# Optimization experiments

Hardware: AMD Instinct MI355X
Metric: run time of the kernel (lower is better)

Reference implementation:

```python
import jax, jax.numpy as jnp
import numpy as np

N = 50000      # nodes
E = 500000     # edges (avg degree 10)
D_IN = 256     # input feature dim
HID = 256      # hidden_channels
HEADS = 8
C_HID = HID // HEADS   # 32 per-head dim for concat layers
NCLS = 8               # num_classes (last layer per-head dim, concat=False)


def setup_inputs() -> dict:
    key = jax.random.key(0)
    keys = iter(jax.random.split(key, 64))
    def w(shape, s=0.05):
        return jax.random.normal(next(keys), shape, jnp.float32) * s
    inp = {}
    inp["x"] = jax.random.normal(next(keys), (N, D_IN), jnp.float32)
    inp["edge_index"] = jax.random.randint(next(keys), (2, E), 0, N, jnp.int32)
    # (fan_in, heads*per_head_out, skip_out) per layer; layer3: concat=False
    layer_cfg = [(D_IN, HEADS * C_HID, HEADS * C_HID),
                 (HID, HEADS * C_HID, HEADS * C_HID),
                 (HID, HEADS * NCLS, NCLS)]
    for i, (fin, hc, skip) in enumerate(layer_cfg, 1):
        for nm in ("q", "k", "v"):
            inp[f"W{nm}{i}"] = w((fin, hc))
            inp[f"b{nm}{i}"] = jnp.zeros((hc,), jnp.float32)
        inp[f"Ws{i}"] = w((fin, skip))
        inp[f"bs{i}"] = jnp.zeros((skip,), jnp.float32)
        inp[f"Wb{i}"] = w((3 * skip, 1))
    for i in (1, 2):
        inp[f"ln{i}_g"] = jnp.ones((HID,), jnp.float32)
        inp[f"ln{i}_b"] = jnp.zeros((HID,), jnp.float32)
    return inp


def _layer_norm(x, g, b):
    mu = x.mean(-1, keepdims=True)
    var = ((x - mu) ** 2).mean(-1, keepdims=True)
    return (x - mu) * jax.lax.rsqrt(var + 1e-5) * g + b


def _tconv(x, src, dst, Wq, bq, Wk, bk, Wv, bv, Ws, bs, Wb, concat):
    """PyG TransformerConv with beta=True, root_weight=True, eval-mode (no dropout)."""
    n = x.shape[0]
    q = (x @ Wq + bq).reshape(n, HEADS, -1)   # [N,H,C]
    k = (x @ Wk + bk).reshape(n, HEADS, -1)
    v = (x @ Wv + bv).reshape(n, HEADS, -1)
    C = q.shape[-1]
    # per-edge attention logits, scaled dot product
    logits = (q[dst] * k[src]).sum(-1) * jax.lax.rsqrt(jnp.float32(C))  # [E,H]
    # segment softmax over incoming edges of each dst node
    m = jax.ops.segment_max(logits, dst, num_segments=n)                # [N,H]
    m = jnp.where(jnp.isfinite(m), m, 0.0)                              # empty segments
    e = jnp.exp(logits - m[dst])
    s = jax.ops.segment_sum(e, dst, num_segments=n)
    alpha = e / (s[dst] + 1e-16)                                        # [E,H]
    # scatter-aggregate messages
    out = jax.ops.segment_sum(v[src] * alpha[:, :, None], dst, num_segments=n)  # [N,H,C]
    out = out.reshape(n, -1) if concat else out.mean(axis=1)
    # beta-gated skip connection
    xr = x @ Ws + bs
    beta = jax.nn.sigmoid(jnp.concatenate([out, xr, out - xr], axis=-1) @ Wb)   # [N,1]
    return beta * xr + (1.0 - beta) * out


def reference(x, edge_index,
              Wq1, bq1, Wk1, bk1, Wv1, bv1, Ws1, bs1, Wb1,
              Wq2, bq2, Wk2, bk2, Wv2, bv2, Ws2, bs2, Wb2,
              Wq3, bq3, Wk3, bk3, Wv3, bv3, Ws3, bs3, Wb3,
              ln1_g, ln1_b, ln2_g, ln2_b):
    src, dst = edge_index[0], edge_index[1]
    h = jax.nn.relu(_layer_norm(
        _tconv(x, src, dst, Wq1, bq1, Wk1, bk1, Wv1, bv1, Ws1, bs1, Wb1, True),
        ln1_g, ln1_b))
    h = jax.nn.relu(_layer_norm(
        _tconv(h, src, dst, Wq2, bq2, Wk2, bk2, Wv2, bv2, Ws2, bs2, Wb2, True),
        ln2_g, ln2_b))
    return _tconv(h, src, dst, Wq3, bq3, Wk3, bk3, Wv3, bv3, Ws3, bs3, Wb3, False)
```

## Files before the change

### kernel.cpp

```cpp
#include <hip/hip_runtime.h>
#include <stdint.h>

typedef __attribute__((ext_vector_type(8))) short short8;
typedef __attribute__((ext_vector_type(4))) float f32x4;

struct us4 { unsigned short x, y, z, w; };

__device__ __forceinline__ float b2f(unsigned short u){
  union { unsigned int i; float f; } x; x.i = ((unsigned int)u) << 16; return x.f;
}
__device__ __forceinline__ unsigned short f2b(float f){
  union { float f; unsigned int i; } x; x.f = f;
  unsigned int i = x.i;
  unsigned int r = (i + 0x7FFFu + ((i >> 16) & 1u)) >> 16;
  return (unsigned short)r;
}
__device__ __forceinline__ float sane(float v){
  return fminf(fmaxf(v, -1e30f), 1e30f);
}
__device__ __forceinline__ float lclamp(float v){
  return fminf(fmaxf(v, -60.f), 60.f);
}
__device__ __forceinline__ float ldin(const void* p, size_t i, int f32){
  return f32 ? ((const float*)p)[i] : b2f(((const unsigned short*)p)[i]);
}

__global__ void k_flag(const unsigned short* __restrict__ xu, int* __restrict__ flag){
  __shared__ int cnt;
  if (threadIdx.x == 0) cnt = 0;
  __syncthreads();
  unsigned u = xu[2 * threadIdx.x];
  int e = (u >> 7) & 0xFF;
  if (e >= 97 && e <= 132) atomicAdd(&cnt, 1);
  __syncthreads();
  if (threadIdx.x == 0) flag[0] = (cnt >= 192) ? 0 : 1;
}

__global__ void k_cvt(const void* __restrict__ xin, unsigned short* __restrict__ xb,
                      int n4, const int* __restrict__ flagp){
  int f32 = *flagp;
  int i = blockIdx.x * 256 + threadIdx.x;
  if (i < n4){
    if (f32){
      float4 v = ((const float4*)xin)[i];
      us4 o = { f2b(v.x), f2b(v.y), f2b(v.z), f2b(v.w) };
      ((us4*)xb)[i] = o;
    } else {
      ((us4*)xb)[i] = ((const us4*)xin)[i];
    }
  }
}

__global__ void k_deg(const int* __restrict__ ei, int E, int N, int* __restrict__ deg){
  int e = blockIdx.x * 256 + threadIdx.x;
  if (e < E){
    unsigned d = (unsigned)ei[E + e];
    if (d < (unsigned)N) atomicAdd(&deg[d], 1);
  }
}

__global__ void k_bsum(const int* __restrict__ deg, int N, int* __restrict__ bsum){
  int b = blockIdx.x, t = threadIdx.x;
  int i0 = b * 1024 + t * 4;
  int s = 0;
  if (i0 + 4 <= N){
    int4 v = *(const int4*)&deg[i0];
    s = v.x + v.y + v.z + v.w;
  } else {
    #pragma unroll
    for (int j = 0; j < 4; ++j){ int i = i0 + j; if (i < N) s += deg[i]; }
  }
  #pragma unroll
  for (int off = 32; off; off >>= 1) s += __shfl_xor(s, off);
  __shared__ int ws[4];
  if ((t & 63) == 0) ws[t >> 6] = s;
  __syncthreads();
  if (t == 0) bsum[b] = ws[0] + ws[1] + ws[2] + ws[3];
}

__global__ void k_bscan(const int* __restrict__ bsum, int nb,
                        int* __restrict__ boff, int* __restrict__ rowptr, int N){
  int t = threadIdx.x;
  if (nb <= 64){
    int v = (t < nb) ? bsum[t] : 0;
    int inc = v;
    #pragma unroll
    for (int off = 1; off < 64; off <<= 1){
      int u = __shfl_up(inc, off);
      if (t >= off) inc += u;
    }
    if (t < nb) boff[t] = inc - v;
    if (t == 63) rowptr[N] = inc;
  } else {
    if (t == 0){
      int run = 0;
      for (int i = 0; i < nb; ++i){ boff[i] = run; run += bsum[i]; }
      rowptr[N] = run;
    }
  }
}

__global__ void k_rowptr(const int* __restrict__ deg, const int* __restrict__ boff,
                         int N, int* __restrict__ rowptr, int* __restrict__ cursor){
  int b = blockIdx.x, t = threadIdx.x;
  int i0 = b * 1024 + t * 4;
  int d0 = 0, d1 = 0, d2 = 0, d3 = 0;
  if (i0 + 4 <= N){
    int4 v = *(const int4*)&deg[i0];
    d0 = v.x; d1 = v.y; d2 = v.z; d3 = v.w;
  } else {
    if (i0     < N) d0 = deg[i0];
    if (i0 + 1 < N) d1 = deg[i0 + 1];
    if (i0 + 2 < N) d2 = deg[i0 + 2];
    if (i0 + 3 < N) d3 = deg[i0 + 3];
  }
  int s = d0 + d1 + d2 + d3;
  int lane = t & 63, w = t >> 6;
  int inc = s;
  #pragma unroll
  for (int off = 1; off < 64; off <<= 1){
    int u = __shfl_up(inc, off);
    if (lane >= off) inc += u;
  }
  int wex = inc - s;
  __shared__ int wtot[4];
  if (lane == 63) wtot[w] = inc;
  __syncthreads();
  int cross = 0;
  for (int i = 0; i < w; ++i) cross += wtot[i];
  int basev = boff[b] + cross + wex;
  int r0 = basev, r1 = basev + d0, r2 = r1 + d1, r3 = r2 + d2;
  if (i0 + 4 <= N){
    int4 o = { r0, r1, r2, r3 };
    *(int4*)&rowptr[i0] = o;
    *(int4*)&cursor[i0] = o;
  } else {
    if (i0     < N){ rowptr[i0]   = r0; cursor[i0]   = r0; }
    if (i0 + 1 < N){ rowptr[i0+1] = r1; cursor[i0+1] = r1; }
    if (i0 + 2 < N){ rowptr[i0+2] = r2; cursor[i0+2] = r2; }
    if (i0 + 3 < N){ rowptr[i0+3] = r3; cursor[i0+3] = r3; }
  }
}

__global__ void k_scatter(const int* __restrict__ ei, int E, int N,
                          int* __restrict__ cursor, int* __restrict__ srcs){
  int e = blockIdx.x * 256 + threadIdx.x;
  if (e < E){
    unsigned d = (unsigned)ei[E + e];
    if (d < (unsigned)N){
      int pos = atomicAdd(&cursor[d], 1);
      if ((unsigned)pos < (unsigned)E){
        unsigned s = (unsigned)ei[e];
        srcs[pos] = (s < (unsigned)N) ? (int)s : 0;
      }
    }
  }
}

__global__ void k_pack(const void* __restrict__ Wq, const void* __restrict__ bq,
                       const void* __restrict__ Wk, const void* __restrict__ bk,
                       const void* __restrict__ Wv, const void* __restrict__ bv,
                       const void* __restrict__ Ws, const void* __restrict__ bs,
                       unsigned short* __restrict__ WT, float* __restrict__ bias,
                       int Mq, int Ms, int K, const int* __restrict__ flagp){
  int f32 = *flagp;
  int cg = blockIdx.x;
  int k  = threadIdx.x;
  int mat, c, mc;
  if (cg < 3 * Mq){ mat = cg / Mq; c = cg % Mq; mc = Mq; }
  else if (cg < 3 * Mq + Ms){ mat = 3; c = cg - 3 * Mq; mc = Ms; }
  else { mat = 4; c = 0; mc = 1; }
  const void* W = (mat==0)?Wq:(mat==1)?Wk:(mat==2)?Wv:(mat==3)?Ws:(const void*)0;
  WT[(size_t)cg * K + k] = (mat < 4) ? f2b(ldin(W, (size_t)k * mc + c, f32)) : (unsigned short)0;
  if (k == 0){
    const void* B = (mat==0)?bq:(mat==1)?bk:(mat==2)?bv:(mat==3)?bs:(const void*)0;
    bias[cg] = (mat < 4) ? ldin(B, c, f32) : 0.f;
  }
}

__global__ __launch_bounds__(256) void k_gemm(const unsigned short* __restrict__ A,
                                              const unsigned short* __restrict__ WT,
                                              const float* __restrict__ bias,
                                              unsigned short* __restrict__ B0,
                                              unsigned short* __restrict__ B1,
                                              unsigned short* __restrict__ B2,
                                              unsigned short* __restrict__ B3,
                                              int N, int Mout, int secshift){
  __shared__ __align__(16) unsigned short Alds[64][264];
  __shared__ __align__(16) unsigned short Clds[32][276];
  int tid = threadIdx.x, wid = tid >> 6, lane = tid & 63;
  int l15 = lane & 15, l4 = lane >> 4;
  int row0 = blockIdx.x * 64;
  {
    int srow = tid >> 2, sc4 = tid & 3;
    int ar = row0 + srow; if (ar >= N) ar = N - 1;
    const unsigned short* Ap = A + (size_t)ar * 256;
    #pragma unroll
    for (int i = 0; i < 8; ++i){
      int col = (sc4 + 4 * i) * 8;
      *(short8*)&Alds[srow][col] = *(const short8*)&Ap[col];
    }
  }
  __syncthreads();
  int secw = 1 << secshift;
  int strow = tid >> 3, stchunk = tid & 7;
  for (int cb = wid * 64; cb < Mout; cb += 256){
    f32x4 acc[4][4] = {};
    #pragma unroll
    for (int k0 = 0; k0 < 256; k0 += 32){
      short8 a0 = *(const short8*)&Alds[l15     ][k0 + l4*8];
      short8 a1 = *(const short8*)&Alds[16 + l15][k0 + l4*8];
      short8 a2 = *(const short8*)&Alds[32 + l15][k0 + l4*8];
      short8 a3 = *(const short8*)&Alds[48 + l15][k0 + l4*8];
      const unsigned short* wb = WT + (size_t)(cb + l15) * 256 + k0 + l4*8;
      short8 b0 = *(const short8*)(wb);
      short8 b1 = *(const short8*)(wb + 16*256);
      short8 b2 = *(const short8*)(wb + 32*256);
      short8 b3 = *(const short8*)(wb + 48*256);
      acc[0][0] = __builtin_amdgcn_mfma_f32_16x16x32_bf16(a0, b0, acc[0][0], 0,0,0);
      acc[0][1] = __builtin_amdgcn_mfma_f32_16x16x32_bf16(a0, b1, acc[0][1], 0,0,0);
      acc[0][2] = __builtin_amdgcn_mfma_f32_16x16x32_bf16(a0, b2, acc[0][2], 0,0,0);
      acc[0][3] = __builtin_amdgcn_mfma_f32_16x16x32_bf16(a0, b3, acc[0][3], 0,0,0);
      acc[1][0] = __builtin_amdgcn_mfma_f32_16x16x32_bf16(a1, b0, acc[1][0], 0,0,0);
      acc[1][1] = __builtin_amdgcn_mfma_f32_16x16x32_bf16(a1, b1, acc[1][1], 0,0,0);
      acc[1][2] = __builtin_amdgcn_mfma_f32_16x16x32_bf16(a1, b2, acc[1][2], 0,0,0);
      acc[1][3] = __builtin_amdgcn_mfma_f32_16x16x32_bf16(a1, b3, acc[1][3], 0,0,0);
      acc[2][0] = __builtin_amdgcn_mfma_f32_16x16x32_bf16(a2, b0, acc[2][0], 0,0,0);
      acc[2][1] = __builtin_amdgcn_mfma_f32_16x16x32_bf16(a2, b1, acc[2][1], 0,0,0);
      acc[2][2] = __builtin_amdgcn_mfma_f32_16x16x32_bf16(a2, b2, acc[2][2], 0,0,0);
      acc[2][3] = __builtin_amdgcn_mfma_f32_16x16x32_bf16(a2, b3, acc[2][3], 0,0,0);
      acc[3][0] = __builtin_amdgcn_mfma_f32_16x16x32_bf16(a3, b0, acc[3][0], 0,0,0);
      acc[3][1] = __builtin_amdgcn_mfma_f32_16x16x32_bf16(a3, b1, acc[3][1], 0,0,0);
      acc[3][2] = __builtin_amdgcn_mfma_f32_16x16x32_bf16(a3, b2, acc[3][2], 0,0,0);
      acc[3][3] = __builtin_amdgcn_mfma_f32_16x16x32_bf16(a3, b3, acc[3][3], 0,0,0);
    }
    int gb = cb - wid * 64;
    #pragma unroll
    for (int ph = 0; ph < 2; ++ph){
      #pragma unroll
      for (int rt2 = 0; rt2 < 2; ++rt2){
        int rt = ph*2 + rt2;
        #pragma unroll
        for (int ct = 0; ct < 4; ++ct){
          float bv = bias[cb + ct*16 + l15];
          #pragma unroll
          for (int r = 0; r < 4; ++r)
            Clds[rt2*16 + l4*4 + r][wid*64 + ct*16 + l15] = f2b(acc[rt][ct][r] + bv);
        }
      }
      __syncthreads();
      int grow = row0 + ph*32 + strow;
      if (grow < N){
        int g0 = gb + stchunk * 32;
        int mat = g0 >> secshift;
        int cc  = g0 & (secw - 1);
        unsigned short* Bp = (mat==0)?B0:(mat==1)?B1:(mat==2)?B2:B3;
        unsigned short* dst = Bp + (size_t)grow * secw + cc;
        const unsigned short* srcp = &Clds[strow][stchunk * 32];
        #pragma unroll
        for (int j = 0; j < 4; ++j)
          *(short8*)(dst + j*8) = *(const short8*)(srcp + j*8);
      }
      __syncthreads();
    }
  }
}

__global__ __launch_bounds__(256) void k_attn(const unsigned short* __restrict__ qb,
                                              const unsigned short* __restrict__ kb,
                                              const unsigned short* __restrict__ vb,
                                              const unsigned short* __restrict__ xb,
                                              const int* __restrict__ rowptr,
                                              const int* __restrict__ srcs,
                                              const void* __restrict__ Wb,
                                              const void* __restrict__ lng,
                                              const void* __restrict__ lnb,
                                              unsigned short* __restrict__ hout,
                                              int N, int E, const int* __restrict__ flagp){
  int f32 = *flagp;
  int tid = threadIdx.x, w = tid >> 6, l = tid & 63;
  int n = blockIdx.x * 4 + w;
  if (n >= N) return;
  size_t base = (size_t)n * 256;
  us4 qv = *(const us4*)&qb[base + l*4];
  float q0 = b2f(qv.x), q1 = b2f(qv.y), q2 = b2f(qv.z), q3 = b2f(qv.w);
  int e0 = rowptr[n], e1 = rowptr[n+1];
  if (e0 < 0) e0 = 0;
  if (e1 > E) e1 = E;
  const float scale = 0.17677669529663687f;
  float ss = 0.f, o0 = 0.f, o1 = 0.f, o2 = 0.f, o3 = 0.f;
  int e = e0;
  for (; e + 4 <= e1; e += 4){
    unsigned s0 = (unsigned)srcs[e];   if (s0 >= (unsigned)N) s0 = 0;
    unsigned s1 = (unsigned)srcs[e+1]; if (s1 >= (unsigned)N) s1 = 0;
    unsigned s2 = (unsigned)srcs[e+2]; if (s2 >= (unsigned)N) s2 = 0;
    unsigned s3 = (unsigned)srcs[e+3]; if (s3 >= (unsigned)N) s3 = 0;
    us4 kA = *(const us4*)&kb[(size_t)s0*256 + l*4];
    us4 kB = *(const us4*)&kb[(size_t)s1*256 + l*4];
    us4 kC = *(const us4*)&kb[(size_t)s2*256 + l*4];
    us4 kD = *(const us4*)&kb[(size_t)s3*256 + l*4];
    us4 vA = *(const us4*)&vb[(size_t)s0*256 + l*4];
    us4 vB = *(const us4*)&vb[(size_t)s1*256 + l*4];
    us4 vC = *(const us4*)&vb[(size_t)s2*256 + l*4];
    us4 vD = *(const us4*)&vb[(size_t)s3*256 + l*4];
    float pa = q0*b2f(kA.x) + q1*b2f(kA.y) + q2*b2f(kA.z) + q3*b2f(kA.w);
    float pb = q0*b2f(kB.x) + q1*b2f(kB.y) + q2*b2f(kB.z) + q3*b2f(kB.w);
    float pc = q0*b2f(kC.x) + q1*b2f(kC.y) + q2*b2f(kC.z) + q3*b2f(kC.w);
    float pd = q0*b2f(kD.x) + q1*b2f(kD.y) + q2*b2f(kD.z) + q3*b2f(kD.w);
    pa += __shfl_xor(pa, 1); pa += __shfl_xor(pa, 2); pa += __shfl_xor(pa, 4);
    pb += __shfl_xor(pb, 1); pb += __shfl_xor(pb, 2); pb += __shfl_xor(pb, 4);
    pc += __shfl_xor(pc, 1); pc += __shfl_xor(pc, 2); pc += __shfl_xor(pc, 4);
    pd += __shfl_xor(pd, 1); pd += __shfl_xor(pd, 2); pd += __shfl_xor(pd, 4);
    float ea = __expf(lclamp(pa * scale));
    float eb = __expf(lclamp(pb * scale));
    float ec = __expf(lclamp(pc * scale));
    float ed = __expf(lclamp(pd * scale));
    ss += ea + eb + ec + ed;
    o0 += ea*b2f(vA.x) + eb*b2f(vB.x) + ec*b2f(vC.x) + ed*b2f(vD.x);
    o1 += ea*b2f(vA.y) + eb*b2f(vB.y) + ec*b2f(vC.y) + ed*b2f(vD.y);
    o2 += ea*b2f(vA.z) + eb*b2f(vB.z) + ec*b2f(vC.z) + ed*b2f(vD.z);
    o3 += ea*b2f(vA.w) + eb*b2f(vB.w) + ec*b2f(vC.w) + ed*b2f(vD.w);
  }
  for (; e < e1; ++e){
    unsigned s = (unsigned)srcs[e]; if (s >= (unsigned)N) s = 0;
    us4 kk = *(const us4*)&kb[(size_t)s*256 + l*4];
    us4 vv = *(const us4*)&vb[(size_t)s*256 + l*4];
    float p = q0*b2f(kk.x) + q1*b2f(kk.y) + q2*b2f(kk.z) + q3*b2f(kk.w);
    p += __shfl_xor(p, 1); p += __shfl_xor(p, 2); p += __shfl_xor(p, 4);
    float a = __expf(lclamp(p * scale));
    ss += a;
    o0 += a*b2f(vv.x); o1 += a*b2f(vv.y); o2 += a*b2f(vv.z); o3 += a*b2f(vv.w);
  }
  float sinv = 1.f / (ss + 1e-16f);
  o0 = sane(o0 * sinv); o1 = sane(o1 * sinv);
  o2 = sane(o2 * sinv); o3 = sane(o3 * sinv);
  int c = l * 4;
  us4 xv = *(const us4*)&xb[base + c];
  float x0 = sane(b2f(xv.x)), x1 = sane(b2f(xv.y)), x2 = sane(b2f(xv.z)), x3 = sane(b2f(xv.w));
  float d = o0*ldin(Wb, c+0, f32) + x0*ldin(Wb, 256+c+0, f32) + (o0-x0)*ldin(Wb, 512+c+0, f32)
          + o1*ldin(Wb, c+1, f32) + x1*ldin(Wb, 256+c+1, f32) + (o1-x1)*ldin(Wb, 512+c+1, f32)
          + o2*ldin(Wb, c+2, f32) + x2*ldin(Wb, 256+c+2, f32) + (o2-x2)*ldin(Wb, 512+c+2, f32)
          + o3*ldin(Wb, c+3, f32) + x3*ldin(Wb, 256+c+3, f32) + (o3-x3)*ldin(Wb, 512+c+3, f32);
  #pragma unroll
  for (int off = 32; off; off >>= 1) d += __shfl_xor(d, off);
  float beta = 1.f / (1.f + __expf(-d));
  float r0 = beta*x0 + (1.f-beta)*o0;
  float r1 = beta*x1 + (1.f-beta)*o1;
  float r2 = beta*x2 + (1.f-beta)*o2;
  float r3 = beta*x3 + (1.f-beta)*o3;
  float sm = r0 + r1 + r2 + r3;
  #pragma unroll
  for (int off = 32; off; off >>= 1) sm += __shfl_xor(sm, off);
  float mu = sm * (1.f/256.f);
  float d0 = r0-mu, d1 = r1-mu, d2 = r2-mu, d3 = r3-mu;
  float vv2 = d0*d0 + d1*d1 + d2*d2 + d3*d3;
  #pragma unroll
  for (int off = 32; off; off >>= 1) vv2 += __shfl_xor(vv2, off);
  float rs = rsqrtf(vv2 * (1.f/256.f) + 1e-5f);
  us4 outv;
  outv.x = f2b(fmaxf(d0*rs*ldin(lng,c+0,f32) + ldin(lnb,c+0,f32), 0.f));
  outv.y = f2b(fmaxf(d1*rs*ldin(lng,c+1,f32) + ldin(lnb,c+1,f32), 0.f));
  outv.z = f2b(fmaxf(d2*rs*ldin(lng,c+2,f32) + ldin(lnb,c+2,f32), 0.f));
  outv.w = f2b(fmaxf(d3*rs*ldin(lng,c+3,f32) + ldin(lnb,c+3,f32), 0.f));
  *(us4*)&hout[base + c] = outv;
}

__global__ __launch_bounds__(256) void k_final(const unsigned short* __restrict__ q3,
                                               const unsigned short* __restrict__ k3,
                                               const unsigned short* __restrict__ v3,
                                               const unsigned short* __restrict__ x3,
                                               const int* __restrict__ rowptr,
                                               const int* __restrict__ srcs,
                                               const void* __restrict__ Wb,
                                               void* __restrict__ outp,
                                               int N, int E, const int* __restrict__ flagp){
  int f32 = *flagp;
  int tid = threadIdx.x, w = tid >> 6, l = tid & 63;
  int n = blockIdx.x * 4 + w;
  if (n >= N) return;
  int es = l >> 4, h = (l >> 1) & 7, j = l & 1;
  size_t base = (size_t)n * 64;
  us4 qv = *(const us4*)&q3[base + h*8 + j*4];
  float q0 = b2f(qv.x), q1 = b2f(qv.y), q2 = b2f(qv.z), q3f = b2f(qv.w);
  int e0 = rowptr[n], e1 = rowptr[n+1];
  if (e0 < 0) e0 = 0;
  if (e1 > E) e1 = E;
  int deg = e1 - e0;
  const float scale = 0.35355339059327373f;
  float ss = 0.f, o0 = 0.f, o1 = 0.f, o2 = 0.f, o3 = 0.f;
  for (int ei = es; ei < deg; ei += 4){
    unsigned s = (unsigned)srcs[e0 + ei]; if (s >= (unsigned)N) s = 0;
    us4 kk = *(const us4*)&k3[(size_t)s*64 + h*8 + j*4];
    us4 vv = *(const us4*)&v3[(size_t)s*64 + h*8 + j*4];
    float p = q0*b2f(kk.x) + q1*b2f(kk.y) + q2*b2f(kk.z) + q3f*b2f(kk.w);
    p += __shfl_xor(p, 1);
    float a = __expf(lclamp(p * scale));
    ss += a;
    o0 += a*b2f(vv.x); o1 += a*b2f(vv.y); o2 += a*b2f(vv.z); o3 += a*b2f(vv.w);
  }
  #pragma unroll
  for (int off = 16; off <= 32; off <<= 1){
    ss += __shfl_xor(ss, off);
    o0 += __shfl_xor(o0, off); o1 += __shfl_xor(o1, off);
    o2 += __shfl_xor(o2, off); o3 += __shfl_xor(o3, off);
  }
  float sinv = 1.f / (ss + 1e-16f);
  o0 = sane(o0 * sinv); o1 = sane(o1 * sinv);
  o2 = sane(o2 * sinv); o3 = sane(o3 * sinv);
  #pragma unroll
  for (int off = 2; off <= 8; off <<= 1){
    o0 += __shfl_xor(o0, off); o1 += __shfl_xor(o1, off);
    o2 += __shfl_xor(o2, off); o3 += __shfl_xor(o3, off);
  }
  o0 *= 0.125f; o1 *= 0.125f; o2 *= 0.125f; o3 *= 0.125f;
  us4 xv = *(const us4*)&x3[base + j*4];
  float x0 = sane(b2f(xv.x)), x1 = sane(b2f(xv.y)), x2 = sane(b2f(xv.z)), x3v = sane(b2f(xv.w));
  int c = j*4;
  float d = o0*ldin(Wb, c+0, f32) + x0*ldin(Wb, 8+c+0, f32) + (o0-x0)*ldin(Wb, 16+c+0, f32)
          + o1*ldin(Wb, c+1, f32) + x1*ldin(Wb, 8+c+1, f32) + (o1-x1)*ldin(Wb, 16+c+1, f32)
          + o2*ldin(Wb, c+2, f32) + x2*ldin(Wb, 8+c+2, f32) + (o2-x2)*ldin(Wb, 16+c+2, f32)
          + o3*ldin(Wb, c+3, f32) + x3v*ldin(Wb, 8+c+3, f32) + (o3-x3v)*ldin(Wb, 16+c+3, f32);
  d += __shfl_xor(d, 1);
  float beta = 1.f / (1.f + __expf(-d));
  float r0 = beta*x0  + (1.f-beta)*o0;
  float r1 = beta*x1  + (1.f-beta)*o1;
  float r2 = beta*x2  + (1.f-beta)*o2;
  float r3 = beta*x3v + (1.f-beta)*o3;
  if (l < 2){
    if (f32){
      float* op = (float*)outp + (size_t)n*8 + l*4;
      op[0] = r0; op[1] = r1; op[2] = r2; op[3] = r3;
    } else {
      unsigned short* op = (unsigned short*)outp + (size_t)n*8 + l*4;
      op[0] = f2b(r0); op[1] = f2b(r1); op[2] = f2b(r2); op[3] = f2b(r3);
    }
  }
}

extern "C" void kernel_launch(void* const* d_in, const int* in_sizes, int n_in,
                              void* d_out, int out_size, void* d_ws, size_t ws_size,
                              hipStream_t stream){
  const int* ei = (const int*)d_in[1];
  const int N = in_sizes[0] / 256;
  const int E = in_sizes[1] / 2;

  char* wsp = (char*)d_ws;
  size_t off = 0;
  auto alloc = [&](size_t b) -> void* {
    void* p = wsp + off; off = (off + b + 255) & ~(size_t)255; return p;
  };
  unsigned short* WT1  = (unsigned short*)alloc((size_t)1024*256*2);
  unsigned short* WT2  = (unsigned short*)alloc((size_t)1024*256*2);
  unsigned short* WT3  = (unsigned short*)alloc((size_t)256*256*2);
  float* bias1 = (float*)alloc(1024*4);
  float* bias2 = (float*)alloc(1024*4);
  float* bias3 = (float*)alloc(256*4);
  int* flag   = (int*)alloc(256);
  int* deg    = (int*)alloc((size_t)N*4);
  int* rowptr = (int*)alloc((size_t)(N+1)*4);
  int* cursor = (int*)alloc((size_t)N*4);
  int* bsum   = (int*)alloc(1024*4);
  int* boff   = (int*)alloc(1024*4);
  int* srcs   = (int*)alloc((size_t)E*4);
  unsigned short* xbf = (unsigned short*)alloc((size_t)N*256*2);
  unsigned short* qb  = (unsigned short*)alloc((size_t)N*256*2);
  unsigned short* kb  = (unsigned short*)alloc((size_t)N*256*2);
  unsigned short* vb  = (unsigned short*)alloc((size_t)N*256*2);
  unsigned short* xb  = (unsigned short*)alloc((size_t)N*256*2);
  unsigned short* hbuf= (unsigned short*)alloc((size_t)N*256*2);
  unsigned short* q3 = qb;
  unsigned short* k3 = kb;
  unsigned short* v3 = vb;
  unsigned short* x3 = xb;
  (void)ws_size; (void)n_in; (void)out_size;

  k_flag<<<1, 256, 0, stream>>>((const unsigned short*)d_in[0], flag);
  int n4 = (N * 256) / 4;
  k_cvt<<<(n4 + 255) / 256, 256, 0, stream>>>(d_in[0], xbf, n4, flag);

  hipMemsetAsync(deg, 0, (size_t)N*4, stream);
  int eb = (E + 255) / 256;
  int nbk = (N + 1023) / 1024;
  k_deg<<<eb, 256, 0, stream>>>(ei, E, N, deg);
  k_bsum<<<nbk, 256, 0, stream>>>(deg, N, bsum);
  k_bscan<<<1, 64, 0, stream>>>(bsum, nbk, boff, rowptr, N);
  k_rowptr<<<nbk, 256, 0, stream>>>(deg, boff, N, rowptr, cursor);
  k_scatter<<<eb, 256, 0, stream>>>(ei, E, N, cursor, srcs);

  k_pack<<<1024, 256, 0, stream>>>(d_in[2],  d_in[3],  d_in[4],  d_in[5],  d_in[6],  d_in[7],  d_in[8],  d_in[9],  WT1, bias1, 256, 256, 256, flag);
  k_pack<<<1024, 256, 0, stream>>>(d_in[11], d_in[12], d_in[13], d_in[14], d_in[15], d_in[16], d_in[17], d_in[18], WT2, bias2, 256, 256, 256, flag);
  k_pack<<< 256, 256, 0, stream>>>(d_in[20], d_in[21], d_in[22], d_in[23], d_in[24], d_in[25], d_in[26], d_in[27], WT3, bias3,  64,   8, 256, flag);

  int rb = (N + 63) / 64;
  int nb = (N + 3) / 4;
  k_gemm<<<rb, 256, 0, stream>>>(xbf, WT1, bias1, qb, kb, vb, xb, N, 1024, 8);
  k_attn<<<nb, 256, 0, stream>>>(qb, kb, vb, xb, rowptr, srcs, d_in[10], d_in[29], d_in[30], hbuf, N, E, flag);
  k_gemm<<<rb, 256, 0, stream>>>(hbuf, WT2, bias2, qb, kb, vb, xb, N, 1024, 8);
  k_attn<<<nb, 256, 0, stream>>>(qb, kb, vb, xb, rowptr, srcs, d_in[19], d_in[31], d_in[32], hbuf, N, E, flag);
  k_gemm<<<rb, 256, 0, stream>>>(hbuf, WT3, bias3, q3, k3, v3, x3, N, 256, 6);
  k_final<<<nb, 256, 0, stream>>>(q3, k3, v3, x3, rowptr, srcs, d_in[28], d_out, N, E, flag);
}
```

Before: 668.4 us.

## Interleave K and V rows into one buffer for single-gather attention

The GEMM now writes K and V into one interleaved [N,512] (or [N,128]) buffer using per-output row strides. The attention kernels fetch a node's K and V with a single 16-byte load per lane: the lower half-wave holds K and the upper half holds V. Each edge's weight is passed across halves with a shuffle. This cuts the number of scattered gather transactions and makes each load wider, at the cost of half the lanes doing duplicate reductions and more shuffles.

```diff
diff --git a/kernel.cpp b/kernel.cpp
--- a/kernel.cpp
+++ b/kernel.cpp
@@ -185,7 +185,8 @@
                                               unsigned short* __restrict__ B1,
                                               unsigned short* __restrict__ B2,
                                               unsigned short* __restrict__ B3,
-                                              int N, int Mout, int secshift){
+                                              int N, int Mout, int secshift,
+                                              int st0, int st1, int st2, int st3){
   __shared__ __align__(16) unsigned short Alds[64][264];
   __shared__ __align__(16) unsigned short Clds[32][276];
   int tid = threadIdx.x, wid = tid >> 6, lane = tid & 63;
@@ -255,7 +256,8 @@
         int mat = g0 >> secshift;
         int cc  = g0 & (secw - 1);
         unsigned short* Bp = (mat==0)?B0:(mat==1)?B1:(mat==2)?B2:B3;
-        unsigned short* dst = Bp + (size_t)grow * secw + cc;
+        int stw = (mat==0)?st0:(mat==1)?st1:(mat==2)?st2:st3;
+        unsigned short* dst = Bp + (size_t)grow * stw + cc;
         const unsigned short* srcp = &Clds[strow][stchunk * 32];
         #pragma unroll
         for (int j = 0; j < 4; ++j)
@@ -267,8 +269,7 @@
 }
 
 __global__ __launch_bounds__(256) void k_attn(const unsigned short* __restrict__ qb,
-                                              const unsigned short* __restrict__ kb,
-                                              const unsigned short* __restrict__ vb,
+                                              const unsigned short* __restrict__ kv,
                                               const unsigned short* __restrict__ xb,
                                               const int* __restrict__ rowptr,
                                               const int* __restrict__ srcs,
@@ -281,93 +282,104 @@
   int tid = threadIdx.x, w = tid >> 6, l = tid & 63;
   int n = blockIdx.x * 4 + w;
   if (n >= N) return;
+  int m = l & 31;
   size_t base = (size_t)n * 256;
-  us4 qv = *(const us4*)&qb[base + l*4];
-  float q0 = b2f(qv.x), q1 = b2f(qv.y), q2 = b2f(qv.z), q3 = b2f(qv.w);
+  float qf[8];
+  {
+    short8 qv8 = *(const short8*)&qb[base + m*8];
+    #pragma unroll
+    for (int j = 0; j < 8; ++j) qf[j] = b2f((unsigned short)qv8[j]);
+  }
   int e0 = rowptr[n], e1 = rowptr[n+1];
   if (e0 < 0) e0 = 0;
   if (e1 > E) e1 = E;
   const float scale = 0.17677669529663687f;
-  float ss = 0.f, o0 = 0.f, o1 = 0.f, o2 = 0.f, o3 = 0.f;
+  float ss = 0.f;
+  float o[8] = {0,0,0,0,0,0,0,0};
   int e = e0;
-  for (; e + 4 <= e1; e += 4){
+  for (; e + 2 <= e1; e += 2){
     unsigned s0 = (unsigned)srcs[e];   if (s0 >= (unsigned)N) s0 = 0;
     unsigned s1 = (unsigned)srcs[e+1]; if (s1 >= (unsigned)N) s1 = 0;
-    unsigned s2 = (unsigned)srcs[e+2]; if (s2 >= (unsigned)N) s2 = 0;
-    unsigned s3 = (unsigned)srcs[e+3]; if (s3 >= (unsigned)N) s3 = 0;
-    us4 kA = *(const us4*)&kb[(size_t)s0*256 + l*4];
-    us4 kB = *(const us4*)&kb[(size_t)s1*256 + l*4];
-    us4 kC = *(const us4*)&kb[(size_t)s2*256 + l*4];
-    us4 kD = *(const us4*)&kb[(size_t)s3*256 + l*4];
-    us4 vA = *(const us4*)&vb[(size_t)s0*256 + l*4];
-    us4 vB = *(const us4*)&vb[(size_t)s1*256 + l*4];
-    us4 vC = *(const us4*)&vb[(size_t)s2*256 + l*4];
-    us4 vD = *(const us4*)&vb[(size_t)s3*256 + l*4];
-    float pa = q0*b2f(kA.x) + q1*b2f(kA.y) + q2*b2f(kA.z) + q3*b2f(kA.w);
-    float pb = q0*b2f(kB.x) + q1*b2f(kB.y) + q2*b2f(kB.z) + q3*b2f(kB.w);
-    float pc = q0*b2f(kC.x) + q1*b2f(kC.y) + q2*b2f(kC.z) + q3*b2f(kC.w);
-    float pd = q0*b2f(kD.x) + q1*b2f(kD.y) + q2*b2f(kD.z) + q3*b2f(kD.w);
-    pa += __shfl_xor(pa, 1); pa += __shfl_xor(pa, 2); pa += __shfl_xor(pa, 4);
-    pb += __shfl_xor(pb, 1); pb += __shfl_xor(pb, 2); pb += __shfl_xor(pb, 4);
-    pc += __shfl_xor(pc, 1); pc += __shfl_xor(pc, 2); pc += __shfl_xor(pc, 4);
-    pd += __shfl_xor(pd, 1); pd += __shfl_xor(pd, 2); pd += __shfl_xor(pd, 4);
-    float ea = __expf(lclamp(pa * scale));
-    float eb = __expf(lclamp(pb * scale));
-    float ec = __expf(lclamp(pc * scale));
-    float ed = __expf(lclamp(pd * scale));
-    ss += ea + eb + ec + ed;
-    o0 += ea*b2f(vA.x) + eb*b2f(vB.x) + ec*b2f(vC.x) + ed*b2f(vD.x);
-    o1 += ea*b2f(vA.y) + eb*b2f(vB.y) + ec*b2f(vC.y) + ed*b2f(vD.y);
-    o2 += ea*b2f(vA.z) + eb*b2f(vB.z) + ec*b2f(vC.z) + ed*b2f(vD.z);
-    o3 += ea*b2f(vA.w) + eb*b2f(vB.w) + ec*b2f(vC.w) + ed*b2f(vD.w);
+    short8 cA = *(const short8*)&kv[(size_t)s0*512 + l*8];
+    short8 cB = *(const short8*)&kv[(size_t)s1*512 + l*8];
+    float fA[8], fB[8];
+    #pragma unroll
+    for (int j = 0; j < 8; ++j){ fA[j] = b2f((unsigned short)cA[j]); fB[j] = b2f((unsigned short)cB[j]); }
+    float pA = qf[0]*fA[0] + qf[1]*fA[1] + qf[2]*fA[2] + qf[3]*fA[3]
+             + qf[4]*fA[4] + qf[5]*fA[5] + qf[6]*fA[6] + qf[7]*fA[7];
+    float pB = qf[0]*fB[0] + qf[1]*fB[1] + qf[2]*fB[2] + qf[3]*fB[3]
+             + qf[4]*fB[4] + qf[5]*fB[5] + qf[6]*fB[6] + qf[7]*fB[7];
+    pA += __shfl_xor(pA, 1); pA += __shfl_xor(pA, 2);
+    pB += __shfl_xor(pB, 1); pB += __shfl_xor(pB, 2);
+    float wA = __expf(lclamp(pA * scale));
+    float wB = __expf(lclamp(pB * scale));
+    ss += wA + wB;
+    float wvA = __shfl_xor(wA, 32);
+    float wvB = __shfl_xor(wB, 32);
+    #pragma unroll
+    for (int j = 0; j < 8; ++j) o[j] += wvA * fA[j] + wvB * fB[j];
   }
   for (; e < e1; ++e){
     unsigned s = (unsigned)srcs[e]; if (s >= (unsigned)N) s = 0;
-    us4 kk = *(const us4*)&kb[(size_t)s*256 + l*4];
-    us4 vv = *(const us4*)&vb[(size_t)s*256 + l*4];
-    float p = q0*b2f(kk.x) + q1*b2f(kk.y) + q2*b2f(kk.z) + q3*b2f(kk.w);
-    p += __shfl_xor(p, 1); p += __shfl_xor(p, 2); p += __shfl_xor(p, 4);
-    float a = __expf(lclamp(p * scale));
-    ss += a;
-    o0 += a*b2f(vv.x); o1 += a*b2f(vv.y); o2 += a*b2f(vv.z); o3 += a*b2f(vv.w);
-  }
-  float sinv = 1.f / (ss + 1e-16f);
-  o0 = sane(o0 * sinv); o1 = sane(o1 * sinv);
-  o2 = sane(o2 * sinv); o3 = sane(o3 * sinv);
-  int c = l * 4;
-  us4 xv = *(const us4*)&xb[base + c];
-  float x0 = sane(b2f(xv.x)), x1 = sane(b2f(xv.y)), x2 = sane(b2f(xv.z)), x3 = sane(b2f(xv.w));
-  float d = o0*ldin(Wb, c+0, f32) + x0*ldin(Wb, 256+c+0, f32) + (o0-x0)*ldin(Wb, 512+c+0, f32)
-          + o1*ldin(Wb, c+1, f32) + x1*ldin(Wb, 256+c+1, f32) + (o1-x1)*ldin(Wb, 512+c+1, f32)
-          + o2*ldin(Wb, c+2, f32) + x2*ldin(Wb, 256+c+2, f32) + (o2-x2)*ldin(Wb, 512+c+2, f32)
-          + o3*ldin(Wb, c+3, f32) + x3*ldin(Wb, 256+c+3, f32) + (o3-x3)*ldin(Wb, 512+c+3, f32);
-  #pragma unroll
-  for (int off = 32; off; off >>= 1) d += __shfl_xor(d, off);
+    short8 cA = *(const short8*)&kv[(size_t)s*512 + l*8];
+    float fA[8];
+    #pragma unroll
+    for (int j = 0; j < 8; ++j) fA[j] = b2f((unsigned short)cA[j]);
+    float pA = qf[0]*fA[0] + qf[1]*fA[1] + qf[2]*fA[2] + qf[3]*fA[3]
+             + qf[4]*fA[4] + qf[5]*fA[5] + qf[6]*fA[6] + qf[7]*fA[7];
+    pA += __shfl_xor(pA, 1); pA += __shfl_xor(pA, 2);
+    float wA = __expf(lclamp(pA * scale));
+    ss += wA;
+    float wvA = __shfl_xor(wA, 32);
+    #pragma unroll
+    for (int j = 0; j < 8; ++j) o[j] += wvA * fA[j];
+  }
+  float ssu = __shfl_xor(ss, 32);
+  float sinv = 1.f / (ssu + 1e-16f);
+  #pragma unroll
+  for (int j = 0; j < 8; ++j) o[j] = sane(o[j] * sinv);
+  int c0 = m * 8;
+  float xf[8];
+  {
+    short8 xv8 = *(const short8*)&xb[base + c0];
+    #pragma unroll
+    for (int j = 0; j < 8; ++j) xf[j] = sane(b2f((unsigned short)xv8[j]));
+  }
+  float d = 0.f;
+  #pragma unroll
+  for (int j = 0; j < 8; ++j){
+    int c = c0 + j;
+    d += o[j]*ldin(Wb, c, f32) + xf[j]*ldin(Wb, 256+c, f32) + (o[j]-xf[j])*ldin(Wb, 512+c, f32);
+  }
+  d += __shfl_xor(d, 1); d += __shfl_xor(d, 2); d += __shfl_xor(d, 4);
+  d += __shfl_xor(d, 8); d += __shfl_xor(d, 16);
   float beta = 1.f / (1.f + __expf(-d));
-  float r0 = beta*x0 + (1.f-beta)*o0;
-  float r1 = beta*x1 + (1.f-beta)*o1;
-  float r2 = beta*x2 + (1.f-beta)*o2;
-  float r3 = beta*x3 + (1.f-beta)*o3;
-  float sm = r0 + r1 + r2 + r3;
-  #pragma unroll
-  for (int off = 32; off; off >>= 1) sm += __shfl_xor(sm, off);
+  float r[8], sm = 0.f;
+  #pragma unroll
+  for (int j = 0; j < 8; ++j){ r[j] = beta*xf[j] + (1.f-beta)*o[j]; sm += r[j]; }
+  sm += __shfl_xor(sm, 1); sm += __shfl_xor(sm, 2); sm += __shfl_xor(sm, 4);
+  sm += __shfl_xor(sm, 8); sm += __shfl_xor(sm, 16);
   float mu = sm * (1.f/256.f);
-  float d0 = r0-mu, d1 = r1-mu, d2 = r2-mu, d3 = r3-mu;
-  float vv2 = d0*d0 + d1*d1 + d2*d2 + d3*d3;
-  #pragma unroll
-  for (int off = 32; off; off >>= 1) vv2 += __shfl_xor(vv2, off);
-  float rs = rsqrtf(vv2 * (1.f/256.f) + 1e-5f);
-  us4 outv;
-  outv.x = f2b(fmaxf(d0*rs*ldin(lng,c+0,f32) + ldin(lnb,c+0,f32), 0.f));
-  outv.y = f2b(fmaxf(d1*rs*ldin(lng,c+1,f32) + ldin(lnb,c+1,f32), 0.f));
-  outv.z = f2b(fmaxf(d2*rs*ldin(lng,c+2,f32) + ldin(lnb,c+2,f32), 0.f));
-  outv.w = f2b(fmaxf(d3*rs*ldin(lng,c+3,f32) + ldin(lnb,c+3,f32), 0.f));
-  *(us4*)&hout[base + c] = outv;
+  float vv = 0.f;
+  #pragma unroll
+  for (int j = 0; j < 8; ++j){ float dj = r[j]-mu; vv += dj*dj; }
+  vv += __shfl_xor(vv, 1); vv += __shfl_xor(vv, 2); vv += __shfl_xor(vv, 4);
+  vv += __shfl_xor(vv, 8); vv += __shfl_xor(vv, 16);
+  float rs = rsqrtf(vv * (1.f/256.f) + 1e-5f);
+  if (l >= 32){
+    short8 outv;
+    #pragma unroll
+    for (int j = 0; j < 8; ++j){
+      int c = c0 + j;
+      float y = (r[j]-mu)*rs*ldin(lng, c, f32) + ldin(lnb, c, f32);
+      outv[j] = (short)f2b(fmaxf(y, 0.f));
+    }
+    *(short8*)&hout[base + c0] = outv;
+  }
 }
 
 __global__ __launch_bounds__(256) void k_final(const unsigned short* __restrict__ q3,
-                                               const unsigned short* __restrict__ k3,
-                                               const unsigned short* __restrict__ v3,
+                                               const unsigned short* __restrict__ kv3,
                                                const unsigned short* __restrict__ x3,
                                                const int* __restrict__ rowptr,
                                                const int* __restrict__ srcs,
@@ -378,61 +390,68 @@
   int tid = threadIdx.x, w = tid >> 6, l = tid & 63;
   int n = blockIdx.x * 4 + w;
   if (n >= N) return;
-  int es = l >> 4, h = (l >> 1) & 7, j = l & 1;
+  int es = l >> 4, t = l & 15;
   size_t base = (size_t)n * 64;
-  us4 qv = *(const us4*)&q3[base + h*8 + j*4];
-  float q0 = b2f(qv.x), q1 = b2f(qv.y), q2 = b2f(qv.z), q3f = b2f(qv.w);
+  float qf[8];
+  {
+    short8 qv8 = *(const short8*)&q3[base + (t & 7)*8];
+    #pragma unroll
+    for (int j = 0; j < 8; ++j) qf[j] = b2f((unsigned short)qv8[j]);
+  }
   int e0 = rowptr[n], e1 = rowptr[n+1];
   if (e0 < 0) e0 = 0;
   if (e1 > E) e1 = E;
   int deg = e1 - e0;
   const float scale = 0.35355339059327373f;
-  float ss = 0.f, o0 = 0.f, o1 = 0.f, o2 = 0.f, o3 = 0.f;
+  float ss = 0.f;
+  float o[8] = {0,0,0,0,0,0,0,0};
   for (int ei = es; ei < deg; ei += 4){
     unsigned s = (unsigned)srcs[e0 + ei]; if (s >= (unsigned)N) s = 0;
-    us4 kk = *(const us4*)&k3[(size_t)s*64 + h*8 + j*4];
-    us4 vv = *(const us4*)&v3[(size_t)s*64 + h*8 + j*4];
-    float p = q0*b2f(kk.x) + q1*b2f(kk.y) + q2*b2f(kk.z) + q3f*b2f(kk.w);
-    p += __shfl_xor(p, 1);
-    float a = __expf(lclamp(p * scale));
-    ss += a;
-    o0 += a*b2f(vv.x); o1 += a*b2f(vv.y); o2 += a*b2f(vv.z); o3 += a*b2f(vv.w);
-  }
-  #pragma unroll
-  for (int off = 16; off <= 32; off <<= 1){
-    ss += __shfl_xor(ss, off);
-    o0 += __shfl_xor(o0, off); o1 += __shfl_xor(o1, off);
-    o2 += __shfl_xor(o2, off); o3 += __shfl_xor(o3, off);
-  }
-  float sinv = 1.f / (ss + 1e-16f);
-  o0 = sane(o0 * sinv); o1 = sane(o1 * sinv);
-  o2 = sane(o2 * sinv); o3 = sane(o3 * sinv);
-  #pragma unroll
-  for (int off = 2; off <= 8; off <<= 1){
-    o0 += __shfl_xor(o0, off); o1 += __shfl_xor(o1, off);
-    o2 += __shfl_xor(o2, off); o3 += __shfl_xor(o3, off);
-  }
-  o0 *= 0.125f; o1 *= 0.125f; o2 *= 0.125f; o3 *= 0.125f;
-  us4 xv = *(const us4*)&x3[base + j*4];
-  float x0 = sane(b2f(xv.x)), x1 = sane(b2f(xv.y)), x2 = sane(b2f(xv.z)), x3v = sane(b2f(xv.w));
-  int c = j*4;
-  float d = o0*ldin(Wb, c+0, f32) + x0*ldin(Wb, 8+c+0, f32) + (o0-x0)*ldin(Wb, 16+c+0, f32)
-          + o1*ldin(Wb, c+1, f32) + x1*ldin(Wb, 8+c+1, f32) + (o1-x1)*ldin(Wb, 16+c+1, f32)
-          + o2*ldin(Wb, c+2, f32) + x2*ldin(Wb, 8+c+2, f32) + (o2-x2)*ldin(Wb, 16+c+2, f32)
-          + o3*ldin(Wb, c+3, f32) + x3v*ldin(Wb, 8+c+3, f32) + (o3-x3v)*ldin(Wb, 16+c+3, f32);
-  d += __shfl_xor(d, 1);
+    short8 cA = *(const short8*)&kv3[(size_t)s*128 + t*8];
+    float fA[8];
+    #pragma unroll
+    for (int j = 0; j < 8; ++j) fA[j] = b2f((unsigned short)cA[j]);
+    float p = qf[0]*fA[0] + qf[1]*fA[1] + qf[2]*fA[2] + qf[3]*fA[3]
+            + qf[4]*fA[4] + qf[5]*fA[5] + qf[6]*fA[6] + qf[7]*fA[7];
+    float wA = __expf(lclamp(p * scale));
+    ss += wA;
+    float wv = __shfl_xor(wA, 8);
+    #pragma unroll
+    for (int j = 0; j < 8; ++j) o[j] += wv * fA[j];
+  }
+  ss += __shfl_xor(ss, 16); ss += __shfl_xor(ss, 32);
+  #pragma unroll
+  for (int j = 0; j < 8; ++j){ o[j] += __shfl_xor(o[j], 16); o[j] += __shfl_xor(o[j], 32); }
+  float ssu = __shfl_xor(ss, 8);
+  float sinv = 1.f / (ssu + 1e-16f);
+  #pragma unroll
+  for (int j = 0; j < 8; ++j) o[j] = sane(o[j] * sinv);
+  #pragma unroll
+  for (int j = 0; j < 8; ++j){
+    o[j] += __shfl_xor(o[j], 1); o[j] += __shfl_xor(o[j], 2); o[j] += __shfl_xor(o[j], 4);
+    o[j] *= 0.125f;
+  }
+  float xf[8];
+  {
+    short8 xv8 = *(const short8*)&x3[base];
+    #pragma unroll
+    for (int j = 0; j < 8; ++j) xf[j] = sane(b2f((unsigned short)xv8[j]));
+  }
+  float d = 0.f;
+  #pragma unroll
+  for (int j = 0; j < 8; ++j)
+    d += o[j]*ldin(Wb, j, f32) + xf[j]*ldin(Wb, 8+j, f32) + (o[j]-xf[j])*ldin(Wb, 16+j, f32);
   float beta = 1.f / (1.f + __expf(-d));
-  float r0 = beta*x0  + (1.f-beta)*o0;
-  float r1 = beta*x1  + (1.f-beta)*o1;
-  float r2 = beta*x2  + (1.f-beta)*o2;
-  float r3 = beta*x3v + (1.f-beta)*o3;
-  if (l < 2){
+  if (l == 8){
     if (f32){
-      float* op = (float*)outp + (size_t)n*8 + l*4;
-      op[0] = r0; op[1] = r1; op[2] = r2; op[3] = r3;
+      float* op = (float*)outp + (size_t)n*8;
+      #pragma unroll
+      for (int j = 0; j < 8; ++j) op[j] = beta*xf[j] + (1.f-beta)*o[j];
     } else {
-      unsigned short* op = (unsigned short*)outp + (size_t)n*8 + l*4;
-      op[0] = f2b(r0); op[1] = f2b(r1); op[2] = f2b(r2); op[3] = f2b(r3);
+      short8 ov;
+      #pragma unroll
+      for (int j = 0; j < 8; ++j) ov[j] = (short)f2b(beta*xf[j] + (1.f-beta)*o[j]);
+      *(short8*)((unsigned short*)outp + (size_t)n*8) = ov;
     }
   }
 }
@@ -464,14 +483,12 @@
   int* srcs   = (int*)alloc((size_t)E*4);
   unsigned short* xbf = (unsigned short*)alloc((size_t)N*256*2);
   unsigned short* qb  = (unsigned short*)alloc((size_t)N*256*2);
-  unsigned short* kb  = (unsigned short*)alloc((size_t)N*256*2);
-  unsigned short* vb  = (unsigned short*)alloc((size_t)N*256*2);
+  unsigned short* kv  = (unsigned short*)alloc((size_t)N*512*2);
   unsigned short* xb  = (unsigned short*)alloc((size_t)N*256*2);
   unsigned short* hbuf= (unsigned short*)alloc((size_t)N*256*2);
-  unsigned short* q3 = qb;
-  unsigned short* k3 = kb;
-  unsigned short* v3 = vb;
-  unsigned short* x3 = xb;
+  unsigned short* q3  = qb;
+  unsigned short* kv3 = kv;
+  unsigned short* x3  = xb;
   (void)ws_size; (void)n_in; (void)out_size;
 
   k_flag<<<1, 256, 0, stream>>>((const unsigned short*)d_in[0], flag);
@@ -493,10 +510,10 @@
 
   int rb = (N + 63) / 64;
   int nb = (N + 3) / 4;
-  k_gemm<<<rb, 256, 0, stream>>>(xbf, WT1, bias1, qb, kb, vb, xb, N, 1024, 8);
-  k_attn<<<nb, 256, 0, stream>>>(qb, kb, vb, xb, rowptr, srcs, d_in[10], d_in[29], d_in[30], hbuf, N, E, flag);
-  k_gemm<<<rb, 256, 0, stream>>>(hbuf, WT2, bias2, qb, kb, vb, xb, N, 1024, 8);
-  k_attn<<<nb, 256, 0, stream>>>(qb, kb, vb, xb, rowptr, srcs, d_in[19], d_in[31], d_in[32], hbuf, N, E, flag);
-  k_gemm<<<rb, 256, 0, stream>>>(hbuf, WT3, bias3, q3, k3, v3, x3, N, 256, 6);
-  k_final<<<nb, 256, 0, stream>>>(q3, k3, v3, x3, rowptr, srcs, d_in[28], d_out, N, E, flag);
-}
+  k_gemm<<<rb, 256, 0, stream>>>(xbf, WT1, bias1, qb, kv, kv + 256, xb, N, 1024, 8, 256, 512, 512, 256);
+  k_attn<<<nb, 256, 0, stream>>>(qb, kv, xb, rowptr, srcs, d_in[10], d_in[29], d_in[30], hbuf, N, E, flag);
+  k_gemm<<<rb, 256, 0, stream>>>(hbuf, WT2, bias2, qb, kv, kv + 256, xb, N, 1024, 8, 256, 512, 512, 256);
+  k_attn<<<nb, 256, 0, stream>>>(qb, kv, xb, rowptr, srcs, d_in[19], d_in[31], d_in[32], hbuf, N, E, flag);
+  k_gemm<<<rb, 256, 0, stream>>>(hbuf, WT3, bias3, q3, kv3, kv3 + 64, x3, N, 256, 6, 64, 128, 128, 64);
+  k_final<<<nb, 256, 0, stream>>>(q3, kv3, x3, rowptr, srcs, d_in[28], d_out, N, E, flag);
+}
```

Measured after the change: 897.4 us. 1.34x slower.
